# Kernel tuning notes

Measured on AMD Instinct MI355X. Metric: run time of the kernel, lower is better.

## Reference

```python
import jax, jax.numpy as jnp
import numpy as np

B, N, D, H, QK, HID = 4, 1024, 1024, 16, 64, 4096
BETA = 1.0 / float(np.sqrt(QK))  # default attn_beta = 1/sqrt(qk_dim)


def setup_inputs() -> dict:
    key = jax.random.key(0)
    k1, k2, k3, k4 = jax.random.split(key, 4)
    x = jax.random.normal(k1, (B, N, D), dtype=jnp.float32)
    scale = 1.0 / float(np.sqrt(D))
    Wq = jax.random.normal(k2, (H, QK, D), dtype=jnp.float32) * scale
    Wk = jax.random.normal(k3, (H, QK, D), dtype=jnp.float32) * scale
    W_hop = jax.random.normal(k4, (D, HID), dtype=jnp.float32) * scale
    return {"x": x, "Wq": Wq, "Wk": Wk, "W_hop": W_hop}


def _energy(x, Wq, Wk, W_hop):
    # Graph energy attention (dense path, no adjacency / mask)
    q = jnp.einsum('bnd,hqd->bhnq', x, Wq)  # [B,H,N,QK]
    k = jnp.einsum('bnd,hqd->bhnq', x, Wk)  # [B,H,N,QK]
    scores = BETA * jnp.einsum('bhnq,bhmq->bhnm', q, k)  # [B,H,N,N]
    e_attn = -(1.0 / BETA) * jnp.sum(jax.nn.logsumexp(scores, axis=-1))
    # Hopfield energy: -1/2 * sum relu(x W)^2
    h = jax.nn.relu(jnp.einsum('bnd,de->bne', x, W_hop))  # [B,N,HID]
    e_hop = -0.5 * jnp.sum(h * h)
    return e_attn + e_hop


def reference(x, Wq, Wk, W_hop):
    # Module returns (grad of energy w.r.t. x, energy) via grad_and_value
    energy, grad = jax.value_and_grad(_energy, argnums=0)(x, Wq, Wk, W_hop)
    return grad, energy
```

## Files before the change

kernel.cpp:

```cpp
#include <hip/hip_runtime.h>
#include <hip/hip_bf16.h>
#include <math.h>

#define BETA 0.125f
#define INV_BETA 8.0f

typedef __attribute__((ext_vector_type(8))) short short8v;
typedef __attribute__((ext_vector_type(4))) float f32x4;
typedef union { short8v v; unsigned short u[8]; } v8u;

#define OFF_XB   0u
#define OFF_WCB  2097152u
#define OFF_WCTB 3145728u
#define OFF_WHB  4194304u
#define OFF_WHTB 6291456u
#define OFF_H    8388608u
#define OFF_QB   16777216u
#define OFF_KB   18874368u
#define OFF_QT   20971520u
#define OFF_KT   23068672u
#define OFF_DQK  25165824u
#define OFF_LSE  29360128u
#define OFF_PL   29425664u
#define OFF_PH   29429760u

__device__ __forceinline__ unsigned short f2b(float f) {
    unsigned u = __float_as_uint(f);
    return (unsigned short)((u + 0x7fffu + ((u >> 16) & 1u)) >> 16);
}

__device__ __forceinline__ void gload_lds16(const unsigned short* g, void* l) {
    __builtin_amdgcn_global_load_lds(
        (const __attribute__((address_space(1))) unsigned int*)g,
        (__attribute__((address_space(3))) unsigned int*)l, 16, 0, 0);
}

__device__ __forceinline__ void xcd_swz(int n, int gx, int& bx, int& by) {
    int id = blockIdx.x;
    int nid = (id & 7) * (n >> 3) + (id >> 3);
    bx = nid % gx;
    by = nid / gx;
}

__global__ __launch_bounds__(256) void k_castall(const float* __restrict__ x,
                                                 const float* __restrict__ Wq,
                                                 const float* __restrict__ Wk,
                                                 const float* __restrict__ Whop,
                                                 unsigned short* __restrict__ XB,
                                                 unsigned short* __restrict__ WCB,
                                                 unsigned short* __restrict__ WHB) {
    int i = blockIdx.x * 256 + threadIdx.x;
    const float* s;
    unsigned short* d;
    int j;
    if (i < 1048576) { s = x; d = XB; j = i; }
    else if (i < 1310720) { s = Wq; d = WCB; j = i - 1048576; }
    else if (i < 1572864) { s = Wk; d = WCB + 1048576; j = i - 1310720; }
    else { s = Whop; d = WHB; j = i - 1572864; }
    float4 v = ((const float4*)s)[j];
    ushort4 o;
    o.x = f2b(v.x); o.y = f2b(v.y); o.z = f2b(v.z); o.w = f2b(v.w);
    ((ushort4*)d)[j] = o;
}

__global__ void k_tall(const float* __restrict__ Wq, const float* __restrict__ Wk,
                       const float* __restrict__ Whop,
                       unsigned short* __restrict__ WCTB, unsigned short* __restrict__ WHTB) {
    __shared__ float t[32][33];
    int bx = blockIdx.x;
    int tx = threadIdx.x, ty = threadIdx.y;
    if (bx < 64) {
        int j0 = bx * 32, d0 = blockIdx.y * 32;
#pragma unroll
        for (int i = 0; i < 4; ++i) {
            int j = j0 + ty + 8 * i;
            const float* src = (j < 1024) ? (Wq + (size_t)j * 1024) : (Wk + (size_t)(j - 1024) * 1024);
            t[ty + 8 * i][tx] = src[d0 + tx];
        }
        __syncthreads();
#pragma unroll
        for (int i = 0; i < 4; ++i)
            WCTB[(size_t)(d0 + ty + 8 * i) * 2048 + j0 + tx] = f2b(t[tx][ty + 8 * i]);
    } else {
        int e0 = (bx - 64) * 32, d0 = blockIdx.y * 32;
#pragma unroll
        for (int i = 0; i < 4; ++i)
            t[ty + 8 * i][tx] = Whop[(size_t)(d0 + ty + 8 * i) * 4096 + e0 + tx];
        __syncthreads();
#pragma unroll
        for (int i = 0; i < 4; ++i)
            WHTB[(size_t)(e0 + ty + 8 * i) * 1024 + d0 + tx] = f2b(t[tx][ty + 8 * i]);
    }
}

template <int MI, int NJ>
__device__ __forceinline__ void gemm_core(const unsigned short* __restrict__ A, int lda,
                                          const unsigned short* __restrict__ Bm, int ldb,
                                          int kdim, int rowBase, int colBase,
                                          unsigned short* ldsA, unsigned short* ldsB,
                                          f32x4 (&acc)[MI][NJ]) {
    const int tid = threadIdx.x, lane = tid & 63;
    const int wv = tid >> 6;
    const int lr = lane & 15, lg = lane >> 4;
    const int wrow = (wv >> 1) * (MI * 16);
    const int wcol = (wv & 1) * (NJ * 16);

    for (int kk = 0; kk < kdim; kk += 64) {
#pragma unroll
        for (int iss = 0; iss < MI; ++iss) {
            int p = iss * 256 + tid;
            int row = p >> 3, c = p & 7, cs = c ^ (row & 7);
            gload_lds16(&A[(size_t)(rowBase + row) * lda + kk + cs * 8], (char*)ldsA + p * 16);
        }
#pragma unroll
        for (int iss = 0; iss < NJ; ++iss) {
            int p = iss * 256 + tid;
            int row = p >> 3, c = p & 7, cs = c ^ (row & 7);
            gload_lds16(&Bm[(size_t)(colBase + row) * ldb + kk + cs * 8], (char*)ldsB + p * 16);
        }
        __syncthreads();
#pragma unroll
        for (int kc = 0; kc < 2; ++kc) {
            short8v av[MI], bv[NJ];
#pragma unroll
            for (int i = 0; i < MI; ++i) {
                int row = wrow + i * 16 + lr;
                av[i] = *(const short8v*)((const char*)ldsA + row * 128 + ((kc * 4 + lg) ^ (row & 7)) * 16);
            }
#pragma unroll
            for (int j = 0; j < NJ; ++j) {
                int row = wcol + j * 16 + lr;
                bv[j] = *(const short8v*)((const char*)ldsB + row * 128 + ((kc * 4 + lg) ^ (row & 7)) * 16);
            }
#pragma unroll
            for (int i = 0; i < MI; ++i)
#pragma unroll
                for (int j = 0; j < NJ; ++j)
                    acc[i][j] = __builtin_amdgcn_mfma_f32_16x16x32_bf16(av[i], bv[j], acc[i][j], 0, 0, 0);
        }
        __syncthreads();
    }
}

#define GEMM_IDX(MI, NJ, BX, BY)                                                 \
    const int tid = threadIdx.x, lane = tid & 63, wv = tid >> 6;                 \
    const int lr = lane & 15, lg = lane >> 4;                                    \
    const int row0 = (BX) * (MI * 32) + (wv >> 1) * (MI * 16);                   \
    const int col0 = (BY) * (NJ * 32) + (wv & 1) * (NJ * 16);                    \
    f32x4 acc[MI][NJ];                                                           \
    _Pragma("unroll") for (int i = 0; i < MI; ++i)                               \
        _Pragma("unroll") for (int j = 0; j < NJ; ++j)                           \
            acc[i][j] = (f32x4){0.f, 0.f, 0.f, 0.f};

__global__ __launch_bounds__(256) void mm_proj(const unsigned short* __restrict__ XB,
                                               const unsigned short* __restrict__ WCB,
                                               unsigned short* __restrict__ Qb,
                                               unsigned short* __restrict__ Kb) {
    __shared__ unsigned short ldsA[64 * 64];
    __shared__ unsigned short ldsB[128 * 64];
    int bx, by;
    xcd_swz(1024, 64, bx, by);
    GEMM_IDX(2, 4, bx, by)
    gemm_core<2, 4>(XB, 1024, WCB, 1024, 1024, bx * 64, by * 128, ldsA, ldsB, acc);
    unsigned short* dst = (col0 < 1024) ? Qb : Kb;
    const int cbase = col0 & 1023;
#pragma unroll
    for (int i = 0; i < 2; ++i)
#pragma unroll
        for (int r = 0; r < 4; ++r) {
            int rg = row0 + i * 16 + lg * 4 + r;
            int bb = rg >> 10, n = rg & 1023;
#pragma unroll
            for (int j = 0; j < 4; ++j) {
                int c = cbase + j * 16 + lr;
                int h = c >> 6, q = c & 63;
                dst[((size_t)(bb * 16 + h) * 1024 + n) * 64 + q] = f2b(acc[i][j][r]);
            }
        }
}

__global__ __launch_bounds__(256) void mm_hopfwd(const unsigned short* __restrict__ XB,
                                                 const unsigned short* __restrict__ WHTB,
                                                 unsigned short* __restrict__ Hn,
                                                 float* __restrict__ PH) {
    __shared__ unsigned short ldsA[128 * 64];
    __shared__ unsigned short ldsB[128 * 64];
    __shared__ float red[4];
    int bx, by;
    xcd_swz(1024, 32, bx, by);
    GEMM_IDX(4, 4, bx, by)
    gemm_core<4, 4>(XB, 1024, WHTB, 1024, 1024, bx * 128, by * 128, ldsA, ldsB, acc);
    float ss = 0.f;
#pragma unroll
    for (int i = 0; i < 4; ++i)
#pragma unroll
        for (int r = 0; r < 4; ++r) {
            size_t rg = row0 + i * 16 + lg * 4 + r;
#pragma unroll
            for (int j = 0; j < 4; ++j) {
                float hv = fmaxf(acc[i][j][r], 0.f);
                ss += hv * hv;
                Hn[rg * 4096 + col0 + j * 16 + lr] = f2b(-hv);
            }
        }
#pragma unroll
    for (int off = 32; off; off >>= 1) ss += __shfl_down(ss, off);
    if (lane == 0) red[wv] = ss;
    __syncthreads();
    if (tid == 0) PH[blockIdx.x] = red[0] + red[1] + red[2] + red[3];
}

__global__ __launch_bounds__(256) void mm_gradall(const unsigned short* __restrict__ Hn,
                                                  const unsigned short* __restrict__ WHB,
                                                  const unsigned short* __restrict__ DQK,
                                                  const unsigned short* __restrict__ WCTB,
                                                  float* __restrict__ out) {
    __shared__ unsigned short ldsA[64 * 64];
    __shared__ unsigned short ldsB[64 * 64];
    int bx, by;
    xcd_swz(1024, 64, bx, by);
    GEMM_IDX(2, 2, bx, by)
    gemm_core<2, 2>(Hn, 4096, WHB, 4096, 4096, bx * 64, by * 64, ldsA, ldsB, acc);
    gemm_core<2, 2>(DQK, 2048, WCTB, 2048, 2048, bx * 64, by * 64, ldsA, ldsB, acc);
#pragma unroll
    for (int i = 0; i < 2; ++i)
#pragma unroll
        for (int r = 0; r < 4; ++r) {
            size_t rg = row0 + i * 16 + lg * 4 + r;
#pragma unroll
            for (int j = 0; j < 2; ++j)
                out[rg * 1024 + col0 + j * 16 + lr] = acc[i][j][r];
        }
}

__global__ __launch_bounds__(256) void k_tqk(const unsigned short* __restrict__ Qb,
                                             const unsigned short* __restrict__ Kb,
                                             unsigned short* __restrict__ QT,
                                             unsigned short* __restrict__ KT) {
    __shared__ unsigned short T[64][65];
    const int z = blockIdx.z;
    const unsigned short* src = z ? Kb : Qb;
    unsigned short* dst = z ? KT : QT;
    const int bh = blockIdx.y;
    const int n0 = blockIdx.x * 64;
    const int t = threadIdx.x;
    {
        int row = t >> 3;
        int colc = (t & 7) * 8;
#pragma unroll
        for (int ii = 0; ii < 2; ++ii) {
            int r = row + 32 * ii;
            v8u vv;
            vv.v = *(const short8v*)&src[((size_t)(bh << 10) + n0 + r) * 64 + colc];
#pragma unroll
            for (int j = 0; j < 8; ++j) T[r][colc + j] = vv.u[j];
        }
    }
    __syncthreads();
    {
        int q = t >> 2;
        int nc = (t & 3) * 16;
        unsigned short buf[16];
#pragma unroll
        for (int j = 0; j < 16; ++j) buf[j] = T[nc + j][q];
        *(short8v*)&dst[((size_t)bh * 64 + q) * 1024 + n0 + nc] = *(short8v*)&buf[0];
        *(short8v*)&dst[((size_t)bh * 64 + q) * 1024 + n0 + nc + 8] = *(short8v*)&buf[8];
    }
}

__global__ __launch_bounds__(256) void k_dq(const unsigned short* __restrict__ Qb,
                                            const unsigned short* __restrict__ Kb,
                                            const unsigned short* __restrict__ KT,
                                            float* __restrict__ LSE,
                                            float* __restrict__ PL,
                                            unsigned short* __restrict__ DQK) {
    __shared__ unsigned short Ktile[2][64 * 64];
    __shared__ unsigned short Ttile[2][64 * 64];
    __shared__ unsigned short P[4][1024];
    int nt, bh;
    xcd_swz(1024, 16, nt, bh);
    const int tid = threadIdx.x, lane = tid & 63, wv = tid >> 6;
    const int nw = nt * 64 + wv * 16;
    const int lr = lane & 15, lg = lane >> 4;
    unsigned short* Pw = &P[wv][0];

    auto stage = [&](int buf, int m0) {
#pragma unroll
        for (int iss = 0; iss < 2; ++iss) {
            int p = iss * 256 + tid;
            int row = p >> 3, c = p & 7, cs = c ^ (row & 7);
            gload_lds16(&Kb[((size_t)(bh << 10) + m0 + row) * 64 + cs * 8],
                        (char*)&Ktile[buf][0] + p * 16);
            gload_lds16(&KT[((size_t)bh * 64 + row) * 1024 + m0 + cs * 8],
                        (char*)&Ttile[buf][0] + p * 16);
        }
    };

    short8v qa[2];
#pragma unroll
    for (int kc = 0; kc < 2; ++kc)
        qa[kc] = *(const short8v*)&Qb[((size_t)(bh << 10) + nw + lr) * 64 + kc * 32 + lg * 8];

    float sm[4];
    f32x4 dq[4];
#pragma unroll
    for (int r = 0; r < 4; ++r) sm[r] = 0.f;
#pragma unroll
    for (int qb = 0; qb < 4; ++qb) dq[qb] = (f32x4){0.f, 0.f, 0.f, 0.f};

    stage(0, 0);
    __syncthreads();
    int buf = 0;
    for (int mt = 0; mt < 16; ++mt) {
        if (mt < 15) stage(buf ^ 1, (mt + 1) * 64);
        const char* Kt = (const char*)&Ktile[buf][0];
        const char* Tt = (const char*)&Ttile[buf][0];
#pragma unroll
        for (int ct = 0; ct < 4; ++ct) {
            int brow = ct * 16 + lr;
            short8v bk0 = *(const short8v*)(Kt + brow * 128 + ((lg) ^ (brow & 7)) * 16);
            short8v bk1 = *(const short8v*)(Kt + brow * 128 + ((lg + 4) ^ (brow & 7)) * 16);
            f32x4 s = {0.f, 0.f, 0.f, 0.f};
            s = __builtin_amdgcn_mfma_f32_16x16x32_bf16(qa[0], bk0, s, 0, 0, 0);
            s = __builtin_amdgcn_mfma_f32_16x16x32_bf16(qa[1], bk1, s, 0, 0, 0);
#pragma unroll
            for (int r = 0; r < 4; ++r) {
                float p = __expf(s[r] * BETA);
                sm[r] += p;
                int row = lg * 4 + r;
                int off = (row * 64 + ct * 16 + lr) ^ ((row & 7) << 3);
                Pw[off] = f2b(p);
            }
        }
        short8v pa[2];
#pragma unroll
        for (int kc = 0; kc < 2; ++kc) {
            int off = (lr * 64 + kc * 32 + lg * 8) ^ ((lr & 7) << 3);
            pa[kc] = *(const short8v*)&Pw[off];
        }
#pragma unroll
        for (int qb = 0; qb < 4; ++qb) {
            int brow = qb * 16 + lr;
            short8v b0 = *(const short8v*)(Tt + brow * 128 + ((lg) ^ (brow & 7)) * 16);
            short8v b1 = *(const short8v*)(Tt + brow * 128 + ((lg + 4) ^ (brow & 7)) * 16);
            dq[qb] = __builtin_amdgcn_mfma_f32_16x16x32_bf16(pa[0], b0, dq[qb], 0, 0, 0);
            dq[qb] = __builtin_amdgcn_mfma_f32_16x16x32_bf16(pa[1], b1, dq[qb], 0, 0, 0);
        }
        __syncthreads();
        buf ^= 1;
    }

#pragma unroll
    for (int off = 1; off < 16; off <<= 1)
#pragma unroll
        for (int r = 0; r < 4; ++r) sm[r] += __shfl_xor(sm[r], off);

    const int b = bh >> 4, h = bh & 15;
#pragma unroll
    for (int r = 0; r < 4; ++r) {
        float inv = 1.0f / sm[r];
#pragma unroll
        for (int qb = 0; qb < 4; ++qb)
            DQK[((size_t)(b << 10) + nw + lg * 4 + r) * 2048 + h * 64 + qb * 16 + lr] =
                f2b(-dq[qb][r] * inv);
    }

    float lsum = 0.f;
    if (lr == 0) {
#pragma unroll
        for (int r = 0; r < 4; ++r) {
            float l = __logf(sm[r]);
            LSE[(size_t)(bh << 10) + nw + lg * 4 + r] = l;
            lsum += l;
        }
    }
    lsum += __shfl_xor(lsum, 16);
    lsum += __shfl_xor(lsum, 32);
    if (lane == 0) PL[(size_t)blockIdx.x * 4 + wv] = lsum;
}

__global__ __launch_bounds__(256) void k_dk(const unsigned short* __restrict__ Qb,
                                            const unsigned short* __restrict__ Kb,
                                            const unsigned short* __restrict__ QT,
                                            const float* __restrict__ LSE,
                                            unsigned short* __restrict__ DQK) {
    __shared__ unsigned short Qtile[2][64 * 64];
    __shared__ unsigned short Ttile[2][64 * 64];
    __shared__ unsigned short P[4][1024];
    int mt, bh;
    xcd_swz(1024, 16, mt, bh);
    const int tid = threadIdx.x, lane = tid & 63, wv = tid >> 6;
    const int mw = mt * 64 + wv * 16;
    const int lr = lane & 15, lg = lane >> 4;
    unsigned short* Pw = &P[wv][0];

    auto stage = [&](int buf, int n0) {
#pragma unroll
        for (int iss = 0; iss < 2; ++iss) {
            int p = iss * 256 + tid;
            int row = p >> 3, c = p & 7, cs = c ^ (row & 7);
            gload_lds16(&Qb[((size_t)(bh << 10) + n0 + row) * 64 + cs * 8],
                        (char*)&Qtile[buf][0] + p * 16);
            gload_lds16(&QT[((size_t)bh * 64 + row) * 1024 + n0 + cs * 8],
                        (char*)&Ttile[buf][0] + p * 16);
        }
    };

    short8v ka[2];
#pragma unroll
    for (int kc = 0; kc < 2; ++kc)
        ka[kc] = *(const short8v*)&Kb[((size_t)(bh << 10) + mw + lr) * 64 + kc * 32 + lg * 8];

    f32x4 dk[4];
#pragma unroll
    for (int qb = 0; qb < 4; ++qb) dk[qb] = (f32x4){0.f, 0.f, 0.f, 0.f};

    stage(0, 0);
    __syncthreads();
    int buf = 0;
    for (int ntl = 0; ntl < 16; ++ntl) {
        const int n0 = ntl * 64;
        float lse_c[4];
#pragma unroll
        for (int ct = 0; ct < 4; ++ct)
            lse_c[ct] = LSE[(size_t)(bh << 10) + n0 + ct * 16 + lr];
        if (ntl < 15) stage(buf ^ 1, n0 + 64);
        const char* Qt = (const char*)&Qtile[buf][0];
        const char* Tt = (const char*)&Ttile[buf][0];
#pragma unroll
        for (int ct = 0; ct < 4; ++ct) {
            int brow = ct * 16 + lr;
            short8v bq0 = *(const short8v*)(Qt + brow * 128 + ((lg) ^ (brow & 7)) * 16);
            short8v bq1 = *(const short8v*)(Qt + brow * 128 + ((lg + 4) ^ (brow & 7)) * 16);
            f32x4 s = {0.f, 0.f, 0.f, 0.f};
            s = __builtin_amdgcn_mfma_f32_16x16x32_bf16(ka[0], bq0, s, 0, 0, 0);
            s = __builtin_amdgcn_mfma_f32_16x16x32_bf16(ka[1], bq1, s, 0, 0, 0);
#pragma unroll
            for (int r = 0; r < 4; ++r) {
                float p = __expf(s[r] * BETA - lse_c[ct]);
                int row = lg * 4 + r;
                int off = (row * 64 + ct * 16 + lr) ^ ((row & 7) << 3);
                Pw[off] = f2b(p);
            }
        }
        short8v pa[2];
#pragma unroll
        for (int kc = 0; kc < 2; ++kc) {
            int off = (lr * 64 + kc * 32 + lg * 8) ^ ((lr & 7) << 3);
            pa[kc] = *(const short8v*)&Pw[off];
        }
#pragma unroll
        for (int qb = 0; qb < 4; ++qb) {
            int brow = qb * 16 + lr;
            short8v b0 = *(const short8v*)(Tt + brow * 128 + ((lg) ^ (brow & 7)) * 16);
            short8v b1 = *(const short8v*)(Tt + brow * 128 + ((lg + 4) ^ (brow & 7)) * 16);
            dk[qb] = __builtin_amdgcn_mfma_f32_16x16x32_bf16(pa[0], b0, dk[qb], 0, 0, 0);
            dk[qb] = __builtin_amdgcn_mfma_f32_16x16x32_bf16(pa[1], b1, dk[qb], 0, 0, 0);
        }
        __syncthreads();
        buf ^= 1;
    }
    const int b = bh >> 4, h = bh & 15;
#pragma unroll
    for (int qb = 0; qb < 4; ++qb)
#pragma unroll
        for (int r = 0; r < 4; ++r)
            DQK[((size_t)(b << 10) + mw + lg * 4 + r) * 2048 + 1024 + h * 64 + qb * 16 + lr] = f2b(-dk[qb][r]);
}

__global__ __launch_bounds__(256) void k_fin(const float* __restrict__ pl,
                                             const float* __restrict__ ph,
                                             float* __restrict__ out) {
    const int tid = threadIdx.x;
    float s1 = 0.f, s2 = 0.f;
    for (int i = tid; i < 4096; i += 256) s1 += pl[i];
    for (int i = tid; i < 1024; i += 256) s2 += ph[i];
#pragma unroll
    for (int off = 32; off; off >>= 1) {
        s1 += __shfl_down(s1, off);
        s2 += __shfl_down(s2, off);
    }
    __shared__ float r1[4], r2[4];
    if ((tid & 63) == 0) { r1[tid >> 6] = s1; r2[tid >> 6] = s2; }
    __syncthreads();
    if (tid == 0) {
        float S1 = r1[0] + r1[1] + r1[2] + r1[3];
        float S2 = r2[0] + r2[1] + r2[2] + r2[3];
        out[(size_t)4194304] = -INV_BETA * S1 - 0.5f * S2;
    }
}

extern "C" void kernel_launch(void* const* d_in, const int* in_sizes, int n_in,
                              void* d_out, int out_size, void* d_ws, size_t ws_size,
                              hipStream_t stream) {
    (void)in_sizes; (void)n_in; (void)out_size; (void)ws_size;
    const float* x    = (const float*)d_in[0];
    const float* Wq   = (const float*)d_in[1];
    const float* Wk   = (const float*)d_in[2];
    const float* Whop = (const float*)d_in[3];
    float* out = (float*)d_out;
    float* ws = (float*)d_ws;

    unsigned short* XB   = (unsigned short*)(ws + OFF_XB);
    unsigned short* WCB  = (unsigned short*)(ws + OFF_WCB);
    unsigned short* WCTB = (unsigned short*)(ws + OFF_WCTB);
    unsigned short* WHB  = (unsigned short*)(ws + OFF_WHB);
    unsigned short* WHTB = (unsigned short*)(ws + OFF_WHTB);
    unsigned short* Hn   = (unsigned short*)(ws + OFF_H);
    unsigned short* Qb   = (unsigned short*)(ws + OFF_QB);
    unsigned short* Kb   = (unsigned short*)(ws + OFF_KB);
    unsigned short* QT   = (unsigned short*)(ws + OFF_QT);
    unsigned short* KT   = (unsigned short*)(ws + OFF_KT);
    unsigned short* DQK  = (unsigned short*)(ws + OFF_DQK);
    float* LSE = ws + OFF_LSE;
    float* PL  = ws + OFF_PL;
    float* PH  = ws + OFF_PH;

    dim3 blk(256);
    k_castall<<<dim3(10240), blk, 0, stream>>>(x, Wq, Wk, Whop, XB, WCB, WHB);
    k_tall<<<dim3(192, 32), dim3(32, 8), 0, stream>>>(Wq, Wk, Whop, WCTB, WHTB);

    mm_proj<<<dim3(1024), blk, 0, stream>>>(XB, WCB, Qb, Kb);
    k_tqk<<<dim3(16, 64, 2), blk, 0, stream>>>(Qb, Kb, QT, KT);
    k_dq<<<dim3(1024), blk, 0, stream>>>(Qb, Kb, KT, LSE, PL, DQK);
    k_dk<<<dim3(1024), blk, 0, stream>>>(Qb, Kb, QT, LSE, DQK);

    mm_hopfwd<<<dim3(1024), blk, 0, stream>>>(XB, WHTB, Hn, PH);
    mm_gradall<<<dim3(1024), blk, 0, stream>>>(Hn, WHB, DQK, WCTB, out);
    k_fin<<<dim3(1), blk, 0, stream>>>(PL, PH, out);
}
```

Before: 330.0 us.

## Merge cast and transpose prep kernels; widen gradall GEMM tiles to 64x128

Combines the cast kernel and the transpose kernel into one launch, with the block id choosing which job a block does. This removes one kernel launch and the gap between them. Also changes the final gradient GEMM to 64x128 output tiles with 2x4 MFMA accumulators per wave, halving the grid to 512 blocks and adding a matching XCD-aware block mapping. Larger tiles raise B-operand reuse but double LDS for B and add accumulator registers, which may cut occupancy. With 512 blocks on 256 CUs, load balance also changes.

Result: no change. 331.7 us (+0.5%).

```diff
diff --git a/kernel.cpp b/kernel.cpp
--- a/kernel.cpp
+++ b/kernel.cpp
@@ -42,35 +42,39 @@
     by = nid / gx;
 }
 
-__global__ __launch_bounds__(256) void k_castall(const float* __restrict__ x,
-                                                 const float* __restrict__ Wq,
-                                                 const float* __restrict__ Wk,
-                                                 const float* __restrict__ Whop,
-                                                 unsigned short* __restrict__ XB,
-                                                 unsigned short* __restrict__ WCB,
-                                                 unsigned short* __restrict__ WHB) {
-    int i = blockIdx.x * 256 + threadIdx.x;
-    const float* s;
-    unsigned short* d;
-    int j;
-    if (i < 1048576) { s = x; d = XB; j = i; }
-    else if (i < 1310720) { s = Wq; d = WCB; j = i - 1048576; }
-    else if (i < 1572864) { s = Wk; d = WCB + 1048576; j = i - 1310720; }
-    else { s = Whop; d = WHB; j = i - 1572864; }
-    float4 v = ((const float4*)s)[j];
-    ushort4 o;
-    o.x = f2b(v.x); o.y = f2b(v.y); o.z = f2b(v.z); o.w = f2b(v.w);
-    ((ushort4*)d)[j] = o;
-}
-
-__global__ void k_tall(const float* __restrict__ Wq, const float* __restrict__ Wk,
-                       const float* __restrict__ Whop,
-                       unsigned short* __restrict__ WCTB, unsigned short* __restrict__ WHTB) {
+__global__ __launch_bounds__(256) void k_prep(const float* __restrict__ x,
+                                              const float* __restrict__ Wq,
+                                              const float* __restrict__ Wk,
+                                              const float* __restrict__ Whop,
+                                              unsigned short* __restrict__ XB,
+                                              unsigned short* __restrict__ WCB,
+                                              unsigned short* __restrict__ WHB,
+                                              unsigned short* __restrict__ WCTB,
+                                              unsigned short* __restrict__ WHTB) {
     __shared__ float t[32][33];
-    int bx = blockIdx.x;
-    int tx = threadIdx.x, ty = threadIdx.y;
+    int id = blockIdx.x;
+    int tid = threadIdx.x;
+    if (id < 10240) {
+        int i = id * 256 + tid;
+        const float* s;
+        unsigned short* d;
+        int j;
+        if (i < 1048576) { s = x; d = XB; j = i; }
+        else if (i < 1310720) { s = Wq; d = WCB; j = i - 1048576; }
+        else if (i < 1572864) { s = Wk; d = WCB + 1048576; j = i - 1310720; }
+        else { s = Whop; d = WHB; j = i - 1572864; }
+        float4 v = ((const float4*)s)[j];
+        ushort4 o;
+        o.x = f2b(v.x); o.y = f2b(v.y); o.z = f2b(v.z); o.w = f2b(v.w);
+        ((ushort4*)d)[j] = o;
+        return;
+    }
+    int id2 = id - 10240;
+    int bx = id2 % 192;
+    int byy = id2 / 192;
+    int tx = tid & 31, ty = tid >> 5;
     if (bx < 64) {
-        int j0 = bx * 32, d0 = blockIdx.y * 32;
+        int j0 = bx * 32, d0 = byy * 32;
 #pragma unroll
         for (int i = 0; i < 4; ++i) {
             int j = j0 + ty + 8 * i;
@@ -82,7 +86,7 @@
         for (int i = 0; i < 4; ++i)
             WCTB[(size_t)(d0 + ty + 8 * i) * 2048 + j0 + tx] = f2b(t[tx][ty + 8 * i]);
     } else {
-        int e0 = (bx - 64) * 32, d0 = blockIdx.y * 32;
+        int e0 = (bx - 64) * 32, d0 = byy * 32;
 #pragma unroll
         for (int i = 0; i < 4; ++i)
             t[ty + 8 * i][tx] = Whop[(size_t)(d0 + ty + 8 * i) * 4096 + e0 + tx];
@@ -216,19 +220,21 @@
                                                   const unsigned short* __restrict__ WCTB,
                                                   float* __restrict__ out) {
     __shared__ unsigned short ldsA[64 * 64];
-    __shared__ unsigned short ldsB[64 * 64];
-    int bx, by;
-    xcd_swz(1024, 64, bx, by);
-    GEMM_IDX(2, 2, bx, by)
-    gemm_core<2, 2>(Hn, 4096, WHB, 4096, 4096, bx * 64, by * 64, ldsA, ldsB, acc);
-    gemm_core<2, 2>(DQK, 2048, WCTB, 2048, 2048, bx * 64, by * 64, ldsA, ldsB, acc);
+    __shared__ unsigned short ldsB[128 * 64];
+    int id = blockIdx.x;
+    int nid = (id & 7) * 64 + (id >> 3);
+    int by = nid & 7;
+    int bx = nid >> 3;
+    GEMM_IDX(2, 4, bx, by)
+    gemm_core<2, 4>(Hn, 4096, WHB, 4096, 4096, bx * 64, by * 128, ldsA, ldsB, acc);
+    gemm_core<2, 4>(DQK, 2048, WCTB, 2048, 2048, bx * 64, by * 128, ldsA, ldsB, acc);
 #pragma unroll
     for (int i = 0; i < 2; ++i)
 #pragma unroll
         for (int r = 0; r < 4; ++r) {
             size_t rg = row0 + i * 16 + lg * 4 + r;
 #pragma unroll
-            for (int j = 0; j < 2; ++j)
+            for (int j = 0; j < 4; ++j)
                 out[rg * 1024 + col0 + j * 16 + lr] = acc[i][j][r];
         }
 }
@@ -517,8 +523,7 @@
     float* PH  = ws + OFF_PH;
 
     dim3 blk(256);
-    k_castall<<<dim3(10240), blk, 0, stream>>>(x, Wq, Wk, Whop, XB, WCB, WHB);
-    k_tall<<<dim3(192, 32), dim3(32, 8), 0, stream>>>(Wq, Wk, Whop, WCTB, WHTB);
+    k_prep<<<dim3(16384), blk, 0, stream>>>(x, Wq, Wk, Whop, XB, WCB, WHB, WCTB, WHTB);
 
     mm_proj<<<dim3(1024), blk, 0, stream>>>(XB, WCB, Qb, Kb);
     k_tqk<<<dim3(16, 64, 2), blk, 0, stream>>>(Qb, Kb, QT, KT);
@@ -526,6 +531,6 @@
     k_dk<<<dim3(1024), blk, 0, stream>>>(Qb, Kb, QT, LSE, DQK);
 
     mm_hopfwd<<<dim3(1024), blk, 0, stream>>>(XB, WHTB, Hn, PH);
-    mm_gradall<<<dim3(1024), blk, 0, stream>>>(Hn, WHB, DQK, WCTB, out);
+    mm_gradall<<<dim3(512), blk, 0, stream>>>(Hn, WHB, DQK, WCTB, out);
     k_fin<<<dim3(1), blk, 0, stream>>>(PL, PH, out);
 }
```
